# Kernel tuning notes

Measured on AMD Instinct MI355X. Metric: run time of the kernel, lower is better.

## Reference

```python
import jax, jax.numpy as jnp
import numpy as np

SEQ_LEN = 64  # config.SEQ_LEN
T, B, N, D = 256, 128, 4, 2
H_HIS, H_INT = 32, 8


def _uniform(key, shape, k):
    return jax.random.uniform(key, shape, jnp.float32, -k, k)


def setup_inputs() -> dict:
    key = jax.random.key(0)
    ks = jax.random.split(key, 12)
    kh = 1.0 / np.sqrt(H_HIS)
    ki = 1.0 / np.sqrt(H_INT)
    ko = 1.0 / np.sqrt(40)
    return {
        "inputs": jax.random.normal(ks[0], (T, B, N, D), jnp.float32),
        # history LSTM (input 2 -> hidden 32), gate order i,f,g,o like torch
        "Wih_his": _uniform(ks[1], (4 * H_HIS, D), kh),
        "Whh_his": _uniform(ks[2], (4 * H_HIS, H_HIS), kh),
        "bih_his": _uniform(ks[3], (4 * H_HIS,), kh),
        "bhh_his": _uniform(ks[4], (4 * H_HIS,), kh),
        # interaction LSTM (input 2 -> hidden 8)
        "Wih_int": _uniform(ks[5], (4 * H_INT, D), ki),
        "Whh_int": _uniform(ks[6], (4 * H_INT, H_INT), ki),
        "bih_int": _uniform(ks[7], (4 * H_INT,), ki),
        "bhh_int": _uniform(ks[8], (4 * H_INT,), ki),
        # output Linear(40 -> 2)
        "W_out": _uniform(ks[9], (2, H_HIS + H_INT), ko),
        "b_out": _uniform(ks[10], (2,), ko),
    }


def _lstm_windows(x_w, valid, Wih, Whh, bih, bhh):
    """Run an LSTM over L steps for T independent windows at once.
    x_w: [L, Tw, B, d]  inputs per step (leading padding for short windows)
    valid: [L, Tw] bool; while False the state is held at zero, which is
    exactly equivalent to starting the window fresh at its first valid step.
    Returns final hidden state h: [Tw, B, H].
    """
    H = Whh.shape[1]
    Tw, Bb = x_w.shape[1], x_w.shape[2]
    b = bih + bhh

    def step(carry, xs):
        h, c = carry
        x, v = xs
        g = x @ Wih.T + h @ Whh.T + b            # [Tw, B, 4H]
        i, f, gg, o = jnp.split(g, 4, axis=-1)
        c_new = jax.nn.sigmoid(f) * c + jax.nn.sigmoid(i) * jnp.tanh(gg)
        h_new = jax.nn.sigmoid(o) * jnp.tanh(c_new)
        m = v[:, None, None]
        return (jnp.where(m, h_new, 0.0), jnp.where(m, c_new, 0.0)), None

    init = (jnp.zeros((Tw, Bb, H), x_w.dtype), jnp.zeros((Tw, Bb, H), x_w.dtype))
    (h, _), _ = jax.lax.scan(step, init, (x_w, valid))
    return h


def reference(inputs, Wih_his, Whh_his, bih_his, bhh_his,
              Wih_int, Whh_int, bih_int, bhh_int, W_out, b_out):
    Tt, Bb, Nn, Dd = inputs.shape
    L = SEQ_LEN
    # window index for output frame t: frames t-L+1 .. t (clipped; invalid masked)
    t = jnp.arange(Tt)[:, None]
    s = jnp.arange(L)[None, :]
    idx = t - (L - 1) + s                      # [T, L]
    valid = (idx >= 0)
    idx_c = jnp.clip(idx, 0, Tt - 1)
    x_his = inputs[:, :, -1, :][idx_c]         # [T, L, B, d] (ego / last node)
    x_int = inputs[:, :, 0, :][idx_c]          # [T, L, B, d] (interaction node)
    x_his = jnp.transpose(x_his, (1, 0, 2, 3))  # [L, T, B, d]
    x_int = jnp.transpose(x_int, (1, 0, 2, 3))
    v = jnp.transpose(valid)                   # [L, T]

    h_his = _lstm_windows(x_his, v, Wih_his, Whh_his, bih_his, bhh_his)  # [T,B,32]
    h_int = _lstm_windows(x_int, v, Wih_int, Whh_int, bih_int, bhh_int)  # [T,B,8]
    emb = jnp.concatenate([h_his, h_int], axis=-1)                       # [T,B,40]
    return emb @ W_out.T + b_out                                         # [T,B,2]
```

## Files before the change

### kernel.cpp

```cpp
#include <hip/hip_runtime.h>


typedef float v4f __attribute__((ext_vector_type(4)));
typedef _Float16 h8v __attribute__((ext_vector_type(8)));

static __device__ __forceinline__ float fexp2(float x) {
    return __builtin_amdgcn_exp2f(x);
}
static __device__ __forceinline__ float frcp(float x) {
    return __builtin_amdgcn_rcpf(x);
}
static __device__ __forceinline__ unsigned short f2h(float f) {
    _Float16 h = (_Float16)f;
    unsigned short u;
    __builtin_memcpy(&u, &h, 2);
    return u;
}
static __device__ __forceinline__ float h2f(unsigned short u) {
    _Float16 h;
    __builtin_memcpy(&h, &u, 2);
    return (float)h;
}

#define LOG2E    1.442695041f
#define TWOLOG2E 2.885390082f
#define H16ONE   0x3C00u

static __device__ __forceinline__ void lstm_unit(
    float Di, float Df, float Dg, float Do, float& c, float& h)
{
    const float ei = fminf(fexp2(Di), 1e12f);
    const float ef = fminf(fexp2(Df), 1e12f);
    const float eg = fminf(fexp2(Dg), 1e12f);
    const float eo = fminf(fexp2(Do), 1e18f);
    const float pi1 = 1.f + ei, pf1 = 1.f + ef, pg1 = 1.f + eg;
    const float p12 = pi1 * pg1;
    const float r3  = frcp(p12 * pf1);
    const float cn  = fmaf(p12, c, (1.f - eg) * pf1) * r3;
    c = cn;
    const float ec = fminf(fexp2(TWOLOG2E * cn), 1e18f);
    h = (ec - 1.f) * frcp((1.f + eo) * (1.f + ec));
}

__global__ __launch_bounds__(256) void prep_kernel(
    const float* __restrict__ Wih_his, const float* __restrict__ Whh_his,
    const float* __restrict__ bih_his, const float* __restrict__ bhh_his,
    const float* __restrict__ Wih_int, const float* __restrict__ Whh_int,
    const float* __restrict__ bih_int, const float* __restrict__ bhh_int,
    float* __restrict__ ws)
{
    const int i = blockIdx.x * 256 + threadIdx.x;
    unsigned short* wsu = reinterpret_cast<unsigned short*>(ws);

    if (i < 4096) {
        const int T = i >> 9, m = (i >> 5) & 15, k = i & 31;
        const int g = T >> 1;
        const int u = ((m >> 2) << 3) + ((T & 1) << 2) + (m & 3);
        const int orig = g * 32 + u;
        const float s = (g == 2) ? -TWOLOG2E : -LOG2E;
        wsu[i] = f2h(Whh_his[orig * 32 + k] * s);
    } else if (i < 8192) {
        const int e = i - 4096;
        const int T = e >> 9, m = (e >> 5) & 15, k = e & 31;
        const int g = T >> 1;
        const int u = ((m >> 2) << 3) + ((T & 1) << 2) + (m & 3);
        const int orig = g * 32 + u;
        const float s = (g == 2) ? -TWOLOG2E : -LOG2E;
        const float w0 = Wih_his[orig * 2] * s;
        const float w1 = Wih_his[orig * 2 + 1] * s;
        const float b  = (bih_his[orig] + bhh_his[orig]) * s;
        unsigned short v = 0;
        switch (k) {
            case 0: v = f2h(w0); break;
            case 1: v = f2h(w1); break;
            case 2: v = f2h(b);  break;
            case 3: v = f2h(w0 - h2f(f2h(w0))); break;
            case 4: v = f2h(w1 - h2f(f2h(w1))); break;
            case 5: v = f2h(b  - h2f(f2h(b)));  break;
            case 6: v = f2h(w0); break;
            case 7: v = f2h(w1); break;
            default: v = 0; break;
        }
        wsu[4096 + e] = v;
    } else if (i < 9216) {
        const int e = i - 8192;
        const int T = e >> 9, m = (e >> 5) & 15, k = e & 31;
        const int q = k >> 3, j = k & 7;
        const int g = 2 * T + ((m & 3) >> 1);
        const int u = 2 * (m >> 2) + (m & 1);
        const int orig = g * 8 + u;
        const float s = (g == 2) ? -TWOLOG2E : -LOG2E;
        unsigned short v = 0;
        if (j < 6) {
            const int col = 2 * q + (j & 1);
            const float w = Whh_int[orig * 8 + col] * s;
            v = (j == 2 || j == 3) ? f2h(w - h2f(f2h(w))) : f2h(w);
        } else {
            const int comp = j & 1;
            if (q <= 1) {
                v = f2h(Wih_int[orig * 2 + comp] * s);
            } else if (q == 2) {
                const float w = Wih_int[orig * 2 + comp] * s;
                v = f2h(w - h2f(f2h(w)));
            } else {
                const float b = (bih_int[orig] + bhh_int[orig]) * s;
                v = (comp == 0) ? f2h(b) : f2h(b - h2f(f2h(b)));
            }
        }
        wsu[8192 + e] = v;
    }
}

__global__ __launch_bounds__(64) void fusedw_kernel(
    const float* __restrict__ inp, const float* __restrict__ ws,
    const float* __restrict__ W_out, const float* __restrict__ b_out,
    float* __restrict__ out)
{
    const int lane = threadIdx.x;
    const int n    = lane & 15;
    const int q    = lane >> 4;
    const int Wd   = blockIdx.x;
    const int t    = Wd >> 3;
    const int bg   = Wd & 7;
    const int nsteps = (t >= 63) ? 64 : (t + 1);
    const int tau0   = (t >= 63) ? (t - 63) : 0;

    const unsigned short* wsu = reinterpret_cast<const unsigned short*>(ws);
    const h8v* wa = reinterpret_cast<const h8v*>(wsu);
    const h8v* wx = reinterpret_cast<const h8v*>(wsu + 4096);
    const h8v* wi = reinterpret_cast<const h8v*>(wsu + 8192);
    h8v AW[8], AX[8], AI[2];
#pragma unroll
    for (int T = 0; T < 8; ++T) {
        AW[T] = wa[T * 64 + n * 4 + q];
        AX[T] = wx[T * 64 + n * 4 + q];
    }
#pragma unroll
    for (int T = 0; T < 2; ++T) AI[T] = wi[T * 64 + n * 4 + q];

    const int chain = bg * 16 + n;
    const float* xb0 = inp + chain * 8;
    float2 xvH = *reinterpret_cast<const float2*>(xb0 + tau0 * 1024 + 6);
    float2 xvI = *reinterpret_cast<const float2*>(xb0 + tau0 * 1024);

    union BU { unsigned u[4]; h8v h; };
    BU bhH; bhH.u[0] = bhH.u[1] = bhH.u[2] = bhH.u[3] = 0;
    BU bhI; bhI.u[0] = bhI.u[1] = bhI.u[2] = bhI.u[3] = 0;
    float cH[8] = {0.f, 0.f, 0.f, 0.f, 0.f, 0.f, 0.f, 0.f};
    float hH[8] = {0.f, 0.f, 0.f, 0.f, 0.f, 0.f, 0.f, 0.f};
    float cI0 = 0.f, cI1 = 0.f, ih0 = 0.f, ih1 = 0.f;

#pragma unroll 2
    for (int s = 0; s < nsteps; ++s) {
        const int sn = (s + 1 < nsteps) ? (s + 1) : (nsteps - 1);
        const float* xr = xb0 + (tau0 + sn) * 1024;
        const float2 xnH = *reinterpret_cast<const float2*>(xr + 6);
        const float2 xnI = *reinterpret_cast<const float2*>(xr);

        BU bx;
        {
            const unsigned short xh = f2h(xvH.x), yh = f2h(xvH.y);
            const unsigned short xl = f2h(xvH.x - h2f(xh));
            const unsigned short yl = f2h(xvH.y - h2f(yh));
            bx.u[0] = ((unsigned)yh << 16) | xh;
            bx.u[1] = ((unsigned)xh << 16) | H16ONE;
            bx.u[2] = (H16ONE << 16) | yh;
            bx.u[3] = ((unsigned)yl << 16) | xl;
            if (q != 0) { bx.u[0] = 0; bx.u[1] = 0; bx.u[2] = 0; bx.u[3] = 0; }
        }
        {
            const unsigned short xh = f2h(xvI.x), yh = f2h(xvI.y);
            const unsigned short xl = f2h(xvI.x - h2f(xh));
            const unsigned short yl = f2h(xvI.y - h2f(yh));
            const unsigned ph = ((unsigned)yh << 16) | xh;
            const unsigned pl = ((unsigned)yl << 16) | xl;
            bhI.u[3] = (q == 3) ? ((H16ONE << 16) | H16ONE)
                                : ((q == 1) ? pl : ph);
        }

        const v4f z = {0.f, 0.f, 0.f, 0.f};

        const v4f E0 = __builtin_amdgcn_mfma_f32_16x16x32_f16(AI[0], bhI.h, z, 0, 0, 0);
        const v4f E1 = __builtin_amdgcn_mfma_f32_16x16x32_f16(AI[1], bhI.h, z, 0, 0, 0);

        v4f D[8];
#pragma unroll
        for (int T = 0; T < 8; ++T) {
            const v4f cx = __builtin_amdgcn_mfma_f32_16x16x32_f16(AX[T], bx.h, z, 0, 0, 0);
            D[T] = __builtin_amdgcn_mfma_f32_16x16x32_f16(AW[T], bhH.h, cx, 0, 0, 0);
        }

        lstm_unit(E0[0], E0[2], E1[0], E1[2], cI0, ih0);
        lstm_unit(E0[1], E0[3], E1[1], E1[3], cI1, ih1);

        {
            const unsigned short hh0 = f2h(ih0), hh1 = f2h(ih1);
            const unsigned short hl0 = f2h(ih0 - h2f(hh0));
            const unsigned short hl1 = f2h(ih1 - h2f(hh1));
            bhI.u[0] = ((unsigned)hh1 << 16) | hh0;
            bhI.u[1] = bhI.u[0];
            bhI.u[2] = ((unsigned)hl1 << 16) | hl0;
        }

#pragma unroll
        for (int hi = 0; hi < 2; ++hi) {
#pragma unroll
            for (int lo = 0; lo < 4; ++lo) {
                const int ww = hi * 4 + lo;
                lstm_unit(D[hi][lo], D[2 + hi][lo], D[4 + hi][lo],
                          D[6 + hi][lo], cH[ww], hH[ww]);
            }
        }
#pragma unroll
        for (int d = 0; d < 4; ++d)
            bhH.u[d] = ((unsigned)f2h(hH[2 * d + 1]) << 16) | f2h(hH[2 * d]);

        xvH = xnH;
        xvI = xnI;
    }

    const v4f w0a = *reinterpret_cast<const v4f*>(W_out + q * 8);
    const v4f w0b = *reinterpret_cast<const v4f*>(W_out + q * 8 + 4);
    const v4f w1a = *reinterpret_cast<const v4f*>(W_out + 40 + q * 8);
    const v4f w1b = *reinterpret_cast<const v4f*>(W_out + 40 + q * 8 + 4);
    float e0 = fmaf(W_out[33 + 2 * q], ih1, W_out[32 + 2 * q] * ih0);
    float e1 = fmaf(W_out[73 + 2 * q], ih1, W_out[72 + 2 * q] * ih0);
#pragma unroll
    for (int j = 0; j < 4; ++j) {
        e0 = fmaf(w0a[j], hH[j], fmaf(w0b[j], hH[4 + j], e0));
        e1 = fmaf(w1a[j], hH[j], fmaf(w1b[j], hH[4 + j], e1));
    }
    e0 += __shfl_xor(e0, 16); e1 += __shfl_xor(e1, 16);
    e0 += __shfl_xor(e0, 32); e1 += __shfl_xor(e1, 32);

    if (lane < 16) {
        float2 o;
        o.x = e0 + b_out[0];
        o.y = e1 + b_out[1];
        reinterpret_cast<float2*>(out)[t * 128 + chain] = o;
    }
}

extern "C" void kernel_launch(void* const* d_in, const int* in_sizes, int n_in,
                              void* d_out, int out_size, void* d_ws, size_t ws_size,
                              hipStream_t stream) {
    const float* inp     = (const float*)d_in[0];
    const float* Wih_his = (const float*)d_in[1];
    const float* Whh_his = (const float*)d_in[2];
    const float* bih_his = (const float*)d_in[3];
    const float* bhh_his = (const float*)d_in[4];
    const float* Wih_int = (const float*)d_in[5];
    const float* Whh_int = (const float*)d_in[6];
    const float* bih_int = (const float*)d_in[7];
    const float* bhh_int = (const float*)d_in[8];
    const float* W_out   = (const float*)d_in[9];
    const float* b_out   = (const float*)d_in[10];
    float* out  = (float*)d_out;
    float* ws   = (float*)d_ws;

    prep_kernel<<<dim3(36), dim3(256), 0, stream>>>(
        Wih_his, Whh_his, bih_his, bhh_his,
        Wih_int, Whh_int, bih_int, bhh_int, ws);

    fusedw_kernel<<<dim3(2048), dim3(64), 0, stream>>>(
        inp, ws, W_out, b_out, out);
}
```

Before: 182.0 us.

## Split history LSTM hidden units across two waves with LDS exchange per step

Each block now uses two wavefronts. Each wave computes half of the 32 history-LSTM hidden units (4 gate tiles instead of 8), and the weight layout in prep is reordered to match. Every step the new hidden state is exchanged through double-buffered shared memory with a barrier. The interaction LSTM runs only on wave 1, and the output projection is reduced across waves through LDS. This halves the per-wave serial MFMA and transcendental chain per step, at the cost of a __syncthreads and LDS round-trip on the recurrent critical path.

```diff
diff --git a/kernel.cpp b/kernel.cpp
--- a/kernel.cpp
+++ b/kernel.cpp
@@ -53,19 +53,17 @@
     unsigned short* wsu = reinterpret_cast<unsigned short*>(ws);
 
     if (i < 4096) {
-        const int T = i >> 9, m = (i >> 5) & 15, k = i & 31;
-        const int g = T >> 1;
-        const int u = ((m >> 2) << 3) + ((T & 1) << 2) + (m & 3);
-        const int orig = g * 32 + u;
-        const float s = (g == 2) ? -TWOLOG2E : -LOG2E;
+        const int T8 = i >> 9, m = (i >> 5) & 15, k = i & 31;
+        const int w = T8 >> 2, Tl = T8 & 3;
+        const int orig = Tl * 32 + w * 16 + m;
+        const float s = (Tl == 2) ? -TWOLOG2E : -LOG2E;
         wsu[i] = f2h(Whh_his[orig * 32 + k] * s);
     } else if (i < 8192) {
         const int e = i - 4096;
-        const int T = e >> 9, m = (e >> 5) & 15, k = e & 31;
-        const int g = T >> 1;
-        const int u = ((m >> 2) << 3) + ((T & 1) << 2) + (m & 3);
-        const int orig = g * 32 + u;
-        const float s = (g == 2) ? -TWOLOG2E : -LOG2E;
+        const int T8 = e >> 9, m = (e >> 5) & 15, k = e & 31;
+        const int w = T8 >> 2, Tl = T8 & 3;
+        const int orig = Tl * 32 + w * 16 + m;
+        const float s = (Tl == 2) ? -TWOLOG2E : -LOG2E;
         const float w0 = Wih_his[orig * 2] * s;
         const float w1 = Wih_his[orig * 2 + 1] * s;
         const float b  = (bih_his[orig] + bhh_his[orig]) * s;
@@ -111,12 +109,17 @@
     }
 }
 
-__global__ __launch_bounds__(64) void fusedw_kernel(
+__global__ __launch_bounds__(128, 4) void fused2_kernel(
     const float* __restrict__ inp, const float* __restrict__ ws,
     const float* __restrict__ W_out, const float* __restrict__ b_out,
     float* __restrict__ out)
 {
-    const int lane = threadIdx.x;
+    __shared__ __align__(16) unsigned char hb[2][1280];
+    __shared__ float2 ebuf[16];
+
+    const int tid  = threadIdx.x;
+    const int w    = tid >> 6;
+    const int lane = tid & 63;
     const int n    = lane & 15;
     const int q    = lane >> 4;
     const int Wd   = blockIdx.x;
@@ -129,11 +132,11 @@
     const h8v* wa = reinterpret_cast<const h8v*>(wsu);
     const h8v* wx = reinterpret_cast<const h8v*>(wsu + 4096);
     const h8v* wi = reinterpret_cast<const h8v*>(wsu + 8192);
-    h8v AW[8], AX[8], AI[2];
-#pragma unroll
-    for (int T = 0; T < 8; ++T) {
-        AW[T] = wa[T * 64 + n * 4 + q];
-        AX[T] = wx[T * 64 + n * 4 + q];
+    h8v AW[4], AX[4], AI[2];
+#pragma unroll
+    for (int Tl = 0; Tl < 4; ++Tl) {
+        AW[Tl] = wa[(w * 4 + Tl) * 64 + n * 4 + q];
+        AX[Tl] = wx[(w * 4 + Tl) * 64 + n * 4 + q];
     }
 #pragma unroll
     for (int T = 0; T < 2; ++T) AI[T] = wi[T * 64 + n * 4 + q];
@@ -144,13 +147,16 @@
     float2 xvI = *reinterpret_cast<const float2*>(xb0 + tau0 * 1024);
 
     union BU { unsigned u[4]; h8v h; };
-    BU bhH; bhH.u[0] = bhH.u[1] = bhH.u[2] = bhH.u[3] = 0;
+    BU bh;  bh.u[0] = bh.u[1] = bh.u[2] = bh.u[3] = 0;
     BU bhI; bhI.u[0] = bhI.u[1] = bhI.u[2] = bhI.u[3] = 0;
-    float cH[8] = {0.f, 0.f, 0.f, 0.f, 0.f, 0.f, 0.f, 0.f};
-    float hH[8] = {0.f, 0.f, 0.f, 0.f, 0.f, 0.f, 0.f, 0.f};
+    float cH[4] = {0.f, 0.f, 0.f, 0.f};
+    float hH[4] = {0.f, 0.f, 0.f, 0.f};
     float cI0 = 0.f, cI1 = 0.f, ih0 = 0.f, ih1 = 0.f;
 
-#pragma unroll 2
+    const int wb = n * 80 + w * 32 + q * 8;
+    const int rb = n * 80 + q * 16;
+
+#pragma unroll 1
     for (int s = 0; s < nsteps; ++s) {
         const int sn = (s + 1 < nsteps) ? (s + 1) : (nsteps - 1);
         const float* xr = xb0 + (tau0 + sn) * 1024;
@@ -168,7 +174,10 @@
             bx.u[3] = ((unsigned)yl << 16) | xl;
             if (q != 0) { bx.u[0] = 0; bx.u[1] = 0; bx.u[2] = 0; bx.u[3] = 0; }
         }
-        {
+
+        const v4f z = {0.f, 0.f, 0.f, 0.f};
+
+        if (w == 1) {
             const unsigned short xh = f2h(xvI.x), yh = f2h(xvI.y);
             const unsigned short xl = f2h(xvI.x - h2f(xh));
             const unsigned short yl = f2h(xvI.y - h2f(yh));
@@ -176,24 +185,10 @@
             const unsigned pl = ((unsigned)yl << 16) | xl;
             bhI.u[3] = (q == 3) ? ((H16ONE << 16) | H16ONE)
                                 : ((q == 1) ? pl : ph);
-        }
-
-        const v4f z = {0.f, 0.f, 0.f, 0.f};
-
-        const v4f E0 = __builtin_amdgcn_mfma_f32_16x16x32_f16(AI[0], bhI.h, z, 0, 0, 0);
-        const v4f E1 = __builtin_amdgcn_mfma_f32_16x16x32_f16(AI[1], bhI.h, z, 0, 0, 0);
-
-        v4f D[8];
-#pragma unroll
-        for (int T = 0; T < 8; ++T) {
-            const v4f cx = __builtin_amdgcn_mfma_f32_16x16x32_f16(AX[T], bx.h, z, 0, 0, 0);
-            D[T] = __builtin_amdgcn_mfma_f32_16x16x32_f16(AW[T], bhH.h, cx, 0, 0, 0);
-        }
-
-        lstm_unit(E0[0], E0[2], E1[0], E1[2], cI0, ih0);
-        lstm_unit(E0[1], E0[3], E1[1], E1[3], cI1, ih1);
-
-        {
+            const v4f E0 = __builtin_amdgcn_mfma_f32_16x16x32_f16(AI[0], bhI.h, z, 0, 0, 0);
+            const v4f E1 = __builtin_amdgcn_mfma_f32_16x16x32_f16(AI[1], bhI.h, z, 0, 0, 0);
+            lstm_unit(E0[0], E0[2], E1[0], E1[2], cI0, ih0);
+            lstm_unit(E0[1], E0[3], E1[1], E1[3], cI1, ih1);
             const unsigned short hh0 = f2h(ih0), hh1 = f2h(ih1);
             const unsigned short hl0 = f2h(ih0 - h2f(hh0));
             const unsigned short hl1 = f2h(ih1 - h2f(hh1));
@@ -202,41 +197,56 @@
             bhI.u[2] = ((unsigned)hl1 << 16) | hl0;
         }
 
-#pragma unroll
-        for (int hi = 0; hi < 2; ++hi) {
-#pragma unroll
-            for (int lo = 0; lo < 4; ++lo) {
-                const int ww = hi * 4 + lo;
-                lstm_unit(D[hi][lo], D[2 + hi][lo], D[4 + hi][lo],
-                          D[6 + hi][lo], cH[ww], hH[ww]);
-            }
-        }
-#pragma unroll
-        for (int d = 0; d < 4; ++d)
-            bhH.u[d] = ((unsigned)f2h(hH[2 * d + 1]) << 16) | f2h(hH[2 * d]);
+        v4f D[4];
+#pragma unroll
+        for (int Tl = 0; Tl < 4; ++Tl) {
+            const v4f cx = __builtin_amdgcn_mfma_f32_16x16x32_f16(AX[Tl], bx.h, z, 0, 0, 0);
+            D[Tl] = __builtin_amdgcn_mfma_f32_16x16x32_f16(AW[Tl], bh.h, cx, 0, 0, 0);
+        }
+
+#pragma unroll
+        for (int r = 0; r < 4; ++r)
+            lstm_unit(D[0][r], D[1][r], D[2][r], D[3][r], cH[r], hH[r]);
+
+        {
+            const unsigned p0 = ((unsigned)f2h(hH[1]) << 16) | f2h(hH[0]);
+            const unsigned p1 = ((unsigned)f2h(hH[3]) << 16) | f2h(hH[2]);
+            *reinterpret_cast<uint2*>(&hb[s & 1][wb]) = make_uint2(p0, p1);
+        }
+        __syncthreads();
+        {
+            const uint4 rv = *reinterpret_cast<const uint4*>(&hb[s & 1][rb]);
+            bh.u[0] = rv.x; bh.u[1] = rv.y; bh.u[2] = rv.z; bh.u[3] = rv.w;
+        }
 
         xvH = xnH;
         xvI = xnI;
     }
 
-    const v4f w0a = *reinterpret_cast<const v4f*>(W_out + q * 8);
-    const v4f w0b = *reinterpret_cast<const v4f*>(W_out + q * 8 + 4);
-    const v4f w1a = *reinterpret_cast<const v4f*>(W_out + 40 + q * 8);
-    const v4f w1b = *reinterpret_cast<const v4f*>(W_out + 40 + q * 8 + 4);
-    float e0 = fmaf(W_out[33 + 2 * q], ih1, W_out[32 + 2 * q] * ih0);
-    float e1 = fmaf(W_out[73 + 2 * q], ih1, W_out[72 + 2 * q] * ih0);
-#pragma unroll
-    for (int j = 0; j < 4; ++j) {
-        e0 = fmaf(w0a[j], hH[j], fmaf(w0b[j], hH[4 + j], e0));
-        e1 = fmaf(w1a[j], hH[j], fmaf(w1b[j], hH[4 + j], e1));
+    const int u0 = w * 16 + q * 4;
+    float e0 = 0.f, e1 = 0.f;
+#pragma unroll
+    for (int r = 0; r < 4; ++r) {
+        e0 = fmaf(W_out[u0 + r],      hH[r], e0);
+        e1 = fmaf(W_out[40 + u0 + r], hH[r], e1);
+    }
+    if (w == 1) {
+        e0 = fmaf(W_out[33 + 2 * q], ih1, fmaf(W_out[32 + 2 * q], ih0, e0));
+        e1 = fmaf(W_out[73 + 2 * q], ih1, fmaf(W_out[72 + 2 * q], ih0, e1));
     }
     e0 += __shfl_xor(e0, 16); e1 += __shfl_xor(e1, 16);
     e0 += __shfl_xor(e0, 32); e1 += __shfl_xor(e1, 32);
 
-    if (lane < 16) {
+    if (w == 1 && lane < 16) {
+        float2 p; p.x = e0; p.y = e1;
+        ebuf[n] = p;
+    }
+    __syncthreads();
+    if (w == 0 && lane < 16) {
+        const float2 p = ebuf[n];
         float2 o;
-        o.x = e0 + b_out[0];
-        o.y = e1 + b_out[1];
+        o.x = e0 + p.x + b_out[0];
+        o.y = e1 + p.y + b_out[1];
         reinterpret_cast<float2*>(out)[t * 128 + chain] = o;
     }
 }
@@ -262,6 +272,6 @@
         Wih_his, Whh_his, bih_his, bhh_his,
         Wih_int, Whh_int, bih_int, bhh_int, ws);
 
-    fusedw_kernel<<<dim3(2048), dim3(64), 0, stream>>>(
+    fused2_kernel<<<dim3(2048), dim3(128), 0, stream>>>(
         inp, ws, W_out, b_out, out);
 }
```

Measured after the change: 177.0 us. 1.03x faster.

## Share one window for the first 64 outputs by emitting readouts every step

Applied to the files above, without the earlier changes.

The 63 short windows (t<63) all start at frame 0, so they are prefixes of the t=63 window. One block per batch group (j==0) now runs the full 64-step chain and writes an output after every step. The other blocks each run one full 64-step window for t>=64. This cuts the grid from 2048 to 1544 blocks and removes the redundant prefix recurrences. Every block now runs a fixed 64 steps with unroll 1, and the j==0 blocks pay a per-step readout and shuffle cost.

```diff
diff --git a/kernel.cpp b/kernel.cpp
--- a/kernel.cpp
+++ b/kernel.cpp
@@ -120,10 +120,10 @@
     const int n    = lane & 15;
     const int q    = lane >> 4;
     const int Wd   = blockIdx.x;
-    const int t    = Wd >> 3;
+    const int j    = Wd >> 3;
     const int bg   = Wd & 7;
-    const int nsteps = (t >= 63) ? 64 : (t + 1);
-    const int tau0   = (t >= 63) ? (t - 63) : 0;
+    const int tau0 = j;
+    const bool readout = (j == 0);
 
     const unsigned short* wsu = reinterpret_cast<const unsigned short*>(ws);
     const h8v* wa = reinterpret_cast<const h8v*>(wsu);
@@ -137,6 +137,14 @@
     }
 #pragma unroll
     for (int T = 0; T < 2; ++T) AI[T] = wi[T * 64 + n * 4 + q];
+
+    const v4f w0a = *reinterpret_cast<const v4f*>(W_out + q * 8);
+    const v4f w0b = *reinterpret_cast<const v4f*>(W_out + q * 8 + 4);
+    const v4f w1a = *reinterpret_cast<const v4f*>(W_out + 40 + q * 8);
+    const v4f w1b = *reinterpret_cast<const v4f*>(W_out + 40 + q * 8 + 4);
+    const float wi0a = W_out[32 + 2 * q], wi0b = W_out[33 + 2 * q];
+    const float wi1a = W_out[72 + 2 * q], wi1b = W_out[73 + 2 * q];
+    const float bo0 = b_out[0], bo1 = b_out[1];
 
     const int chain = bg * 16 + n;
     const float* xb0 = inp + chain * 8;
@@ -150,9 +158,9 @@
     float hH[8] = {0.f, 0.f, 0.f, 0.f, 0.f, 0.f, 0.f, 0.f};
     float cI0 = 0.f, cI1 = 0.f, ih0 = 0.f, ih1 = 0.f;
 
-#pragma unroll 2
-    for (int s = 0; s < nsteps; ++s) {
-        const int sn = (s + 1 < nsteps) ? (s + 1) : (nsteps - 1);
+#pragma unroll 1
+    for (int s = 0; s < 64; ++s) {
+        const int sn = (s < 63) ? (s + 1) : 63;
         const float* xr = xb0 + (tau0 + sn) * 1024;
         const float2 xnH = *reinterpret_cast<const float2*>(xr + 6);
         const float2 xnI = *reinterpret_cast<const float2*>(xr);
@@ -215,29 +223,45 @@
         for (int d = 0; d < 4; ++d)
             bhH.u[d] = ((unsigned)f2h(hH[2 * d + 1]) << 16) | f2h(hH[2 * d]);
 
+        if (readout) {
+            float e0 = fmaf(wi0b, ih1, wi0a * ih0);
+            float e1 = fmaf(wi1b, ih1, wi1a * ih0);
+#pragma unroll
+            for (int jj = 0; jj < 4; ++jj) {
+                e0 = fmaf(w0a[jj], hH[jj], fmaf(w0b[jj], hH[4 + jj], e0));
+                e1 = fmaf(w1a[jj], hH[jj], fmaf(w1b[jj], hH[4 + jj], e1));
+            }
+            e0 += __shfl_xor(e0, 16); e1 += __shfl_xor(e1, 16);
+            e0 += __shfl_xor(e0, 32); e1 += __shfl_xor(e1, 32);
+            if (lane < 16) {
+                float2 o;
+                o.x = e0 + bo0;
+                o.y = e1 + bo1;
+                reinterpret_cast<float2*>(out)[s * 128 + chain] = o;
+            }
+        }
+
         xvH = xnH;
         xvI = xnI;
     }
 
-    const v4f w0a = *reinterpret_cast<const v4f*>(W_out + q * 8);
-    const v4f w0b = *reinterpret_cast<const v4f*>(W_out + q * 8 + 4);
-    const v4f w1a = *reinterpret_cast<const v4f*>(W_out + 40 + q * 8);
-    const v4f w1b = *reinterpret_cast<const v4f*>(W_out + 40 + q * 8 + 4);
-    float e0 = fmaf(W_out[33 + 2 * q], ih1, W_out[32 + 2 * q] * ih0);
-    float e1 = fmaf(W_out[73 + 2 * q], ih1, W_out[72 + 2 * q] * ih0);
-#pragma unroll
-    for (int j = 0; j < 4; ++j) {
-        e0 = fmaf(w0a[j], hH[j], fmaf(w0b[j], hH[4 + j], e0));
-        e1 = fmaf(w1a[j], hH[j], fmaf(w1b[j], hH[4 + j], e1));
-    }
-    e0 += __shfl_xor(e0, 16); e1 += __shfl_xor(e1, 16);
-    e0 += __shfl_xor(e0, 32); e1 += __shfl_xor(e1, 32);
-
-    if (lane < 16) {
-        float2 o;
-        o.x = e0 + b_out[0];
-        o.y = e1 + b_out[1];
-        reinterpret_cast<float2*>(out)[t * 128 + chain] = o;
+    if (!readout) {
+        float e0 = fmaf(wi0b, ih1, wi0a * ih0);
+        float e1 = fmaf(wi1b, ih1, wi1a * ih0);
+#pragma unroll
+        for (int jj = 0; jj < 4; ++jj) {
+            e0 = fmaf(w0a[jj], hH[jj], fmaf(w0b[jj], hH[4 + jj], e0));
+            e1 = fmaf(w1a[jj], hH[jj], fmaf(w1b[jj], hH[4 + jj], e1));
+        }
+        e0 += __shfl_xor(e0, 16); e1 += __shfl_xor(e1, 16);
+        e0 += __shfl_xor(e0, 32); e1 += __shfl_xor(e1, 32);
+
+        if (lane < 16) {
+            float2 o;
+            o.x = e0 + bo0;
+            o.y = e1 + bo1;
+            reinterpret_cast<float2*>(out)[(63 + j) * 128 + chain] = o;
+        }
     }
 }
 
@@ -262,6 +286,6 @@
         Wih_his, Whh_his, bih_his, bhh_his,
         Wih_int, Whh_int, bih_int, bhh_int, ws);
 
-    fusedw_kernel<<<dim3(2048), dim3(64), 0, stream>>>(
+    fusedw_kernel<<<dim3(1544), dim3(64), 0, stream>>>(
         inp, ws, W_out, b_out, out);
 }
```

Measured after the change: 176.5 us (median of 2 runs). 1.03x faster.

## Share prefix windows via readout chain and run two LSTM chains per wave

Applied to the files above, without the earlier changes.

Drops the separate short-window blocks for t<63. The window starting at frame 0 is run once and its hidden state is projected and stored after every step, which covers all prefix outputs. Each wave now interleaves two independent 64-step chains (772 blocks instead of 2048), overlapping MFMA and transcendental latency across chains. The cost is doubled register pressure (launch bounds 64,1) and a per-step readout branch in the prefix blocks.

```diff
diff --git a/kernel.cpp b/kernel.cpp
--- a/kernel.cpp
+++ b/kernel.cpp
@@ -40,6 +40,30 @@
     c = cn;
     const float ec = fminf(fexp2(TWOLOG2E * cn), 1e18f);
     h = (ec - 1.f) * frcp((1.f + eo) * (1.f + ec));
+}
+
+static __device__ __forceinline__ void project_store(
+    const float* __restrict__ W_out, const float* __restrict__ b_out,
+    float* __restrict__ out, const float hH[8], float ih0, float ih1,
+    int q, int lane, int outIdx)
+{
+    float e0 = fmaf(W_out[33 + 2 * q], ih1, W_out[32 + 2 * q] * ih0);
+    float e1 = fmaf(W_out[73 + 2 * q], ih1, W_out[72 + 2 * q] * ih0);
+#pragma unroll
+    for (int r = 0; r < 4; ++r) {
+        e0 = fmaf(W_out[q * 8 + r], hH[r],
+                  fmaf(W_out[q * 8 + 4 + r], hH[4 + r], e0));
+        e1 = fmaf(W_out[40 + q * 8 + r], hH[r],
+                  fmaf(W_out[44 + q * 8 + r], hH[4 + r], e1));
+    }
+    e0 += __shfl_xor(e0, 16); e1 += __shfl_xor(e1, 16);
+    e0 += __shfl_xor(e0, 32); e1 += __shfl_xor(e1, 32);
+    if (lane < 16) {
+        float2 o;
+        o.x = e0 + b_out[0];
+        o.y = e1 + b_out[1];
+        reinterpret_cast<float2*>(out)[outIdx] = o;
+    }
 }
 
 __global__ __launch_bounds__(256) void prep_kernel(
@@ -111,7 +135,7 @@
     }
 }
 
-__global__ __launch_bounds__(64) void fusedw_kernel(
+__global__ __launch_bounds__(64, 1) void fusedp_kernel(
     const float* __restrict__ inp, const float* __restrict__ ws,
     const float* __restrict__ W_out, const float* __restrict__ b_out,
     float* __restrict__ out)
@@ -119,11 +143,11 @@
     const int lane = threadIdx.x;
     const int n    = lane & 15;
     const int q    = lane >> 4;
-    const int Wd   = blockIdx.x;
-    const int t    = Wd >> 3;
-    const int bg   = Wd & 7;
-    const int nsteps = (t >= 63) ? 64 : (t + 1);
-    const int tau0   = (t >= 63) ? (t - 63) : 0;
+    const int b    = blockIdx.x;
+    const int id2  = b + 772;
+    const int j1   = b >> 3,  bg1 = b & 7;
+    const int j2   = id2 >> 3, bg2 = id2 & 7;
+    const bool readout = (j1 == 0);
 
     const unsigned short* wsu = reinterpret_cast<const unsigned short*>(ws);
     const h8v* wa = reinterpret_cast<const h8v*>(wsu);
@@ -138,107 +162,154 @@
 #pragma unroll
     for (int T = 0; T < 2; ++T) AI[T] = wi[T * 64 + n * 4 + q];
 
-    const int chain = bg * 16 + n;
-    const float* xb0 = inp + chain * 8;
-    float2 xvH = *reinterpret_cast<const float2*>(xb0 + tau0 * 1024 + 6);
-    float2 xvI = *reinterpret_cast<const float2*>(xb0 + tau0 * 1024);
+    const int chain1 = bg1 * 16 + n;
+    const int chain2 = bg2 * 16 + n;
+    const float* xb1 = inp + chain1 * 8;
+    const float* xb2 = inp + chain2 * 8;
+    float2 xvH1 = *reinterpret_cast<const float2*>(xb1 + j1 * 1024 + 6);
+    float2 xvI1 = *reinterpret_cast<const float2*>(xb1 + j1 * 1024);
+    float2 xvH2 = *reinterpret_cast<const float2*>(xb2 + j2 * 1024 + 6);
+    float2 xvI2 = *reinterpret_cast<const float2*>(xb2 + j2 * 1024);
 
     union BU { unsigned u[4]; h8v h; };
-    BU bhH; bhH.u[0] = bhH.u[1] = bhH.u[2] = bhH.u[3] = 0;
-    BU bhI; bhI.u[0] = bhI.u[1] = bhI.u[2] = bhI.u[3] = 0;
-    float cH[8] = {0.f, 0.f, 0.f, 0.f, 0.f, 0.f, 0.f, 0.f};
-    float hH[8] = {0.f, 0.f, 0.f, 0.f, 0.f, 0.f, 0.f, 0.f};
-    float cI0 = 0.f, cI1 = 0.f, ih0 = 0.f, ih1 = 0.f;
-
-#pragma unroll 2
-    for (int s = 0; s < nsteps; ++s) {
-        const int sn = (s + 1 < nsteps) ? (s + 1) : (nsteps - 1);
-        const float* xr = xb0 + (tau0 + sn) * 1024;
-        const float2 xnH = *reinterpret_cast<const float2*>(xr + 6);
-        const float2 xnI = *reinterpret_cast<const float2*>(xr);
-
-        BU bx;
-        {
-            const unsigned short xh = f2h(xvH.x), yh = f2h(xvH.y);
-            const unsigned short xl = f2h(xvH.x - h2f(xh));
-            const unsigned short yl = f2h(xvH.y - h2f(yh));
-            bx.u[0] = ((unsigned)yh << 16) | xh;
-            bx.u[1] = ((unsigned)xh << 16) | H16ONE;
-            bx.u[2] = (H16ONE << 16) | yh;
-            bx.u[3] = ((unsigned)yl << 16) | xl;
-            if (q != 0) { bx.u[0] = 0; bx.u[1] = 0; bx.u[2] = 0; bx.u[3] = 0; }
-        }
-        {
-            const unsigned short xh = f2h(xvI.x), yh = f2h(xvI.y);
-            const unsigned short xl = f2h(xvI.x - h2f(xh));
-            const unsigned short yl = f2h(xvI.y - h2f(yh));
+    BU bhH1; bhH1.u[0] = bhH1.u[1] = bhH1.u[2] = bhH1.u[3] = 0;
+    BU bhI1; bhI1.u[0] = bhI1.u[1] = bhI1.u[2] = bhI1.u[3] = 0;
+    BU bhH2; bhH2.u[0] = bhH2.u[1] = bhH2.u[2] = bhH2.u[3] = 0;
+    BU bhI2; bhI2.u[0] = bhI2.u[1] = bhI2.u[2] = bhI2.u[3] = 0;
+    float cH1[8] = {0.f, 0.f, 0.f, 0.f, 0.f, 0.f, 0.f, 0.f};
+    float hH1[8] = {0.f, 0.f, 0.f, 0.f, 0.f, 0.f, 0.f, 0.f};
+    float cH2[8] = {0.f, 0.f, 0.f, 0.f, 0.f, 0.f, 0.f, 0.f};
+    float hH2[8] = {0.f, 0.f, 0.f, 0.f, 0.f, 0.f, 0.f, 0.f};
+    float cI01 = 0.f, cI11 = 0.f, ih01 = 0.f, ih11 = 0.f;
+    float cI02 = 0.f, cI12 = 0.f, ih02 = 0.f, ih12 = 0.f;
+
+#pragma unroll 1
+    for (int s = 0; s < 64; ++s) {
+        const int sn = (s < 63) ? (s + 1) : 63;
+        const float* xr1 = xb1 + (j1 + sn) * 1024;
+        const float* xr2 = xb2 + (j2 + sn) * 1024;
+        const float2 xnH1 = *reinterpret_cast<const float2*>(xr1 + 6);
+        const float2 xnI1 = *reinterpret_cast<const float2*>(xr1);
+        const float2 xnH2 = *reinterpret_cast<const float2*>(xr2 + 6);
+        const float2 xnI2 = *reinterpret_cast<const float2*>(xr2);
+
+        BU bx1, bx2;
+        {
+            const unsigned short xh = f2h(xvH1.x), yh = f2h(xvH1.y);
+            const unsigned short xl = f2h(xvH1.x - h2f(xh));
+            const unsigned short yl = f2h(xvH1.y - h2f(yh));
+            bx1.u[0] = ((unsigned)yh << 16) | xh;
+            bx1.u[1] = ((unsigned)xh << 16) | H16ONE;
+            bx1.u[2] = (H16ONE << 16) | yh;
+            bx1.u[3] = ((unsigned)yl << 16) | xl;
+            if (q != 0) { bx1.u[0] = 0; bx1.u[1] = 0; bx1.u[2] = 0; bx1.u[3] = 0; }
+        }
+        {
+            const unsigned short xh = f2h(xvH2.x), yh = f2h(xvH2.y);
+            const unsigned short xl = f2h(xvH2.x - h2f(xh));
+            const unsigned short yl = f2h(xvH2.y - h2f(yh));
+            bx2.u[0] = ((unsigned)yh << 16) | xh;
+            bx2.u[1] = ((unsigned)xh << 16) | H16ONE;
+            bx2.u[2] = (H16ONE << 16) | yh;
+            bx2.u[3] = ((unsigned)yl << 16) | xl;
+            if (q != 0) { bx2.u[0] = 0; bx2.u[1] = 0; bx2.u[2] = 0; bx2.u[3] = 0; }
+        }
+        {
+            const unsigned short xh = f2h(xvI1.x), yh = f2h(xvI1.y);
+            const unsigned short xl = f2h(xvI1.x - h2f(xh));
+            const unsigned short yl = f2h(xvI1.y - h2f(yh));
             const unsigned ph = ((unsigned)yh << 16) | xh;
             const unsigned pl = ((unsigned)yl << 16) | xl;
-            bhI.u[3] = (q == 3) ? ((H16ONE << 16) | H16ONE)
-                                : ((q == 1) ? pl : ph);
+            bhI1.u[3] = (q == 3) ? ((H16ONE << 16) | H16ONE)
+                                 : ((q == 1) ? pl : ph);
+        }
+        {
+            const unsigned short xh = f2h(xvI2.x), yh = f2h(xvI2.y);
+            const unsigned short xl = f2h(xvI2.x - h2f(xh));
+            const unsigned short yl = f2h(xvI2.y - h2f(yh));
+            const unsigned ph = ((unsigned)yh << 16) | xh;
+            const unsigned pl = ((unsigned)yl << 16) | xl;
+            bhI2.u[3] = (q == 3) ? ((H16ONE << 16) | H16ONE)
+                                 : ((q == 1) ? pl : ph);
         }
 
         const v4f z = {0.f, 0.f, 0.f, 0.f};
 
-        const v4f E0 = __builtin_amdgcn_mfma_f32_16x16x32_f16(AI[0], bhI.h, z, 0, 0, 0);
-        const v4f E1 = __builtin_amdgcn_mfma_f32_16x16x32_f16(AI[1], bhI.h, z, 0, 0, 0);
-
-        v4f D[8];
+        const v4f E10 = __builtin_amdgcn_mfma_f32_16x16x32_f16(AI[0], bhI1.h, z, 0, 0, 0);
+        const v4f E11 = __builtin_amdgcn_mfma_f32_16x16x32_f16(AI[1], bhI1.h, z, 0, 0, 0);
+        const v4f E20 = __builtin_amdgcn_mfma_f32_16x16x32_f16(AI[0], bhI2.h, z, 0, 0, 0);
+        const v4f E21 = __builtin_amdgcn_mfma_f32_16x16x32_f16(AI[1], bhI2.h, z, 0, 0, 0);
+
+        v4f D1[8], D2[8];
 #pragma unroll
         for (int T = 0; T < 8; ++T) {
-            const v4f cx = __builtin_amdgcn_mfma_f32_16x16x32_f16(AX[T], bx.h, z, 0, 0, 0);
-            D[T] = __builtin_amdgcn_mfma_f32_16x16x32_f16(AW[T], bhH.h, cx, 0, 0, 0);
-        }
-
-        lstm_unit(E0[0], E0[2], E1[0], E1[2], cI0, ih0);
-        lstm_unit(E0[1], E0[3], E1[1], E1[3], cI1, ih1);
-
-        {
-            const unsigned short hh0 = f2h(ih0), hh1 = f2h(ih1);
-            const unsigned short hl0 = f2h(ih0 - h2f(hh0));
-            const unsigned short hl1 = f2h(ih1 - h2f(hh1));
-            bhI.u[0] = ((unsigned)hh1 << 16) | hh0;
-            bhI.u[1] = bhI.u[0];
-            bhI.u[2] = ((unsigned)hl1 << 16) | hl0;
-        }
-
-#pragma unroll
-        for (int hi = 0; hi < 2; ++hi) {
+            const v4f cx = __builtin_amdgcn_mfma_f32_16x16x32_f16(AX[T], bx1.h, z, 0, 0, 0);
+            D1[T] = __builtin_amdgcn_mfma_f32_16x16x32_f16(AW[T], bhH1.h, cx, 0, 0, 0);
+        }
+#pragma unroll
+        for (int T = 0; T < 8; ++T) {
+            const v4f cx = __builtin_amdgcn_mfma_f32_16x16x32_f16(AX[T], bx2.h, z, 0, 0, 0);
+            D2[T] = __builtin_amdgcn_mfma_f32_16x16x32_f16(AW[T], bhH2.h, cx, 0, 0, 0);
+        }
+
+        lstm_unit(E10[0], E10[2], E11[0], E11[2], cI01, ih01);
+        lstm_unit(E10[1], E10[3], E11[1], E11[3], cI11, ih11);
+        {
+            const unsigned short hh0 = f2h(ih01), hh1 = f2h(ih11);
+            const unsigned short hl0 = f2h(ih01 - h2f(hh0));
+            const unsigned short hl1 = f2h(ih11 - h2f(hh1));
+            bhI1.u[0] = ((unsigned)hh1 << 16) | hh0;
+            bhI1.u[1] = bhI1.u[0];
+            bhI1.u[2] = ((unsigned)hl1 << 16) | hl0;
+        }
+        lstm_unit(E20[0], E20[2], E21[0], E21[2], cI02, ih02);
+        lstm_unit(E20[1], E20[3], E21[1], E21[3], cI12, ih12);
+        {
+            const unsigned short hh0 = f2h(ih02), hh1 = f2h(ih12);
+            const unsigned short hl0 = f2h(ih02 - h2f(hh0));
+            const unsigned short hl1 = f2h(ih12 - h2f(hh1));
+            bhI2.u[0] = ((unsigned)hh1 << 16) | hh0;
+            bhI2.u[1] = bhI2.u[0];
+            bhI2.u[2] = ((unsigned)hl1 << 16) | hl0;
+        }
+
+#pragma unroll
+        for (int hi = 0; hi < 2; ++hi)
 #pragma unroll
             for (int lo = 0; lo < 4; ++lo) {
                 const int ww = hi * 4 + lo;
-                lstm_unit(D[hi][lo], D[2 + hi][lo], D[4 + hi][lo],
-                          D[6 + hi][lo], cH[ww], hH[ww]);
+                lstm_unit(D1[hi][lo], D1[2 + hi][lo], D1[4 + hi][lo],
+                          D1[6 + hi][lo], cH1[ww], hH1[ww]);
             }
-        }
 #pragma unroll
         for (int d = 0; d < 4; ++d)
-            bhH.u[d] = ((unsigned)f2h(hH[2 * d + 1]) << 16) | f2h(hH[2 * d]);
-
-        xvH = xnH;
-        xvI = xnI;
-    }
-
-    const v4f w0a = *reinterpret_cast<const v4f*>(W_out + q * 8);
-    const v4f w0b = *reinterpret_cast<const v4f*>(W_out + q * 8 + 4);
-    const v4f w1a = *reinterpret_cast<const v4f*>(W_out + 40 + q * 8);
-    const v4f w1b = *reinterpret_cast<const v4f*>(W_out + 40 + q * 8 + 4);
-    float e0 = fmaf(W_out[33 + 2 * q], ih1, W_out[32 + 2 * q] * ih0);
-    float e1 = fmaf(W_out[73 + 2 * q], ih1, W_out[72 + 2 * q] * ih0);
-#pragma unroll
-    for (int j = 0; j < 4; ++j) {
-        e0 = fmaf(w0a[j], hH[j], fmaf(w0b[j], hH[4 + j], e0));
-        e1 = fmaf(w1a[j], hH[j], fmaf(w1b[j], hH[4 + j], e1));
-    }
-    e0 += __shfl_xor(e0, 16); e1 += __shfl_xor(e1, 16);
-    e0 += __shfl_xor(e0, 32); e1 += __shfl_xor(e1, 32);
-
-    if (lane < 16) {
-        float2 o;
-        o.x = e0 + b_out[0];
-        o.y = e1 + b_out[1];
-        reinterpret_cast<float2*>(out)[t * 128 + chain] = o;
-    }
+            bhH1.u[d] = ((unsigned)f2h(hH1[2 * d + 1]) << 16) | f2h(hH1[2 * d]);
+
+#pragma unroll
+        for (int hi = 0; hi < 2; ++hi)
+#pragma unroll
+            for (int lo = 0; lo < 4; ++lo) {
+                const int ww = hi * 4 + lo;
+                lstm_unit(D2[hi][lo], D2[2 + hi][lo], D2[4 + hi][lo],
+                          D2[6 + hi][lo], cH2[ww], hH2[ww]);
+            }
+#pragma unroll
+        for (int d = 0; d < 4; ++d)
+            bhH2.u[d] = ((unsigned)f2h(hH2[2 * d + 1]) << 16) | f2h(hH2[2 * d]);
+
+        if (readout)
+            project_store(W_out, b_out, out, hH1, ih01, ih11,
+                          q, lane, s * 128 + chain1);
+
+        xvH1 = xnH1; xvI1 = xnI1;
+        xvH2 = xnH2; xvI2 = xnI2;
+    }
+
+    if (!readout)
+        project_store(W_out, b_out, out, hH1, ih01, ih11,
+                      q, lane, (63 + j1) * 128 + chain1);
+    project_store(W_out, b_out, out, hH2, ih02, ih12,
+                  q, lane, (63 + j2) * 128 + chain2);
 }
 
 extern "C" void kernel_launch(void* const* d_in, const int* in_sizes, int n_in,
@@ -262,6 +333,6 @@
         Wih_his, Whh_his, bih_his, bhh_his,
         Wih_int, Whh_int, bih_int, bhh_int, ws);
 
-    fusedw_kernel<<<dim3(2048), dim3(64), 0, stream>>>(
+    fusedp_kernel<<<dim3(772), dim3(64), 0, stream>>>(
         inp, ws, W_out, b_out, out);
 }
```

Measured after the change: 188.4 us. +3.5%, slower.
